# Performance work log

Hardware: AMD Instinct MI355X
Metric: run time of the kernel (lower is better)

## Reference

```python
import jax, jax.numpy as jnp
import numpy as np

B, D, O = 8192, 64, 256

def setup_inputs() -> dict:
    key = jax.random.key(0)
    k1, k2, k3 = jax.random.split(key, 3)
    x = jax.random.normal(k1, (B, D), dtype=jnp.float32)
    centers = jax.random.uniform(k2, (O, 1, D), dtype=jnp.float32)  # RandomUniform(0,1)
    # Original uses Constant(10.0) which saturates exp(-quad) to 0; use small random
    # betas so the quadratic form is in a numerically meaningful range.
    betas = jax.random.normal(k3, (O, D, D), dtype=jnp.float32) * 0.05
    return {"x": x, "centers": centers, "betas": betas}

def reference(x, centers, betas):
    # precision[o] = betas[o] @ betas[o]^T   -> [O, D, D]
    precision = jnp.einsum('ode,ofe->odf', betas, betas)
    # diff[o,b,:] = centers[o] - x[b]        -> [O, B, D]
    diff = centers - x[None, :, :]
    # quad[o,b] = diff[o,b]^T P[o] diff[o,b] -> [O, B]
    quad = jnp.einsum('obd,odf,obf->ob', diff, precision, diff)
    return jnp.exp(-quad).T  # [B, O]
```

## Files before the change

### kernel.cpp

```cpp
#include <hip/hip_runtime.h>
#include <hip/hip_bf16.h>

typedef __bf16 bf16x8 __attribute__((ext_vector_type(8)));
typedef __bf16 bf16x4 __attribute__((ext_vector_type(4)));
typedef float  f32x4  __attribute__((ext_vector_type(4)));

constexpr int Bn = 8192, Dn = 64, On = 256;

__global__ void k_prep_beta(const float* __restrict__ betas, const float* __restrict__ centers,
                            __bf16* __restrict__ bT, float* __restrict__ ncproj) {
    __shared__ float s[64 * 65];
    const int o = blockIdx.x, tid = threadIdx.x;
    const float* bo = betas + (size_t)o * 4096;
    for (int j = tid; j < 1024; j += 256) {
        int d = j >> 4, e = (j & 15) * 4;
        float4 v = ((const float4*)bo)[j];
        s[d * 65 + e + 0] = v.x; s[d * 65 + e + 1] = v.y;
        s[d * 65 + e + 2] = v.z; s[d * 65 + e + 3] = v.w;
    }
    __syncthreads();
    for (int j = tid; j < 1024; j += 256) {
        int e = j >> 4, d = (j & 15) * 4;
        bf16x4 r;
        r[0] = (__bf16)s[(d + 0) * 65 + e]; r[1] = (__bf16)s[(d + 1) * 65 + e];
        r[2] = (__bf16)s[(d + 2) * 65 + e]; r[3] = (__bf16)s[(d + 3) * 65 + e];
        *(bf16x4*)(bT + (size_t)o * 4096 + e * 64 + d) = r;
    }
    if (tid < 64) {
        float acc = 0.f;
        for (int d = 0; d < 64; ++d) acc += s[d * 65 + tid] * centers[o * 64 + d];
        ncproj[o * 64 + tid] = -acc;
    }
}

__global__ __launch_bounds__(256, 4) void k_main(const float* __restrict__ x,
                                                 const __bf16* __restrict__ bT,
                                                 const float* __restrict__ ncproj,
                                                 float* __restrict__ out) {
    __shared__ __align__(16) unsigned char smem[256 * 144];
    __bf16* sX = (__bf16*)smem;
    float*  sQ = (float*)smem;

    const int tid  = threadIdx.x;
    const int w    = tid >> 6, lane = tid & 63;
    const int col  = lane & 15, grp = lane >> 4;
    const int bbase = blockIdx.x * 256;
    const int o     = blockIdx.y * 4 + w;

    const __bf16* bo = bT + (size_t)o * 4096 + (size_t)col * 64 + grp * 8;
    const float*  cp = ncproj + o * 64 + grp * 4;
    bf16x8 A[4][2];
    f32x4  ncp[4];
#pragma unroll
    for (int mi = 0; mi < 4; ++mi) {
        A[mi][0] = *(const bf16x8*)(bo + mi * 16 * 64);
        A[mi][1] = *(const bf16x8*)(bo + mi * 16 * 64 + 32);
        ncp[mi]  = *(const f32x4*)(cp + mi * 16);
    }

#pragma unroll
    for (int it = 0; it < 16; ++it) {
        int i = it * 256 + tid;
        int row = i >> 4, q4 = i & 15;
        float4 v = ((const float4*)(x + (size_t)(bbase + row) * 64))[q4];
        bf16x4 r;
        r[0] = (__bf16)v.x; r[1] = (__bf16)v.y; r[2] = (__bf16)v.z; r[3] = (__bf16)v.w;
        *(bf16x4*)(sX + row * 72 + q4 * 4) = r;
    }
    __syncthreads();

    float qp[16];
#pragma unroll
    for (int n = 0; n < 16; ++n) {
        const __bf16* xr = sX + (n * 16 + col) * 72 + grp * 8;
        bf16x8 x0 = *(const bf16x8*)(xr);
        bf16x8 x1 = *(const bf16x8*)(xr + 32);
        f32x4 qv = {0.f, 0.f, 0.f, 0.f};
#pragma unroll
        for (int mi = 0; mi < 4; ++mi) {
            f32x4 acc = ncp[mi];
            acc = __builtin_amdgcn_mfma_f32_16x16x32_bf16(A[mi][0], x0, acc, 0, 0, 0);
            acc = __builtin_amdgcn_mfma_f32_16x16x32_bf16(A[mi][1], x1, acc, 0, 0, 0);
            qv += acc * acc;
        }
        qp[n] = (qv[0] + qv[1]) + (qv[2] + qv[3]);
    }
    __syncthreads();

#pragma unroll
    for (int n = 0; n < 16; ++n)
        sQ[(n * 16 + col) * 20 + w * 4 + grp] = qp[n];
    __syncthreads();

    const float* qr = sQ + tid * 20;
    f32x4 r;
#pragma unroll
    for (int j = 0; j < 4; ++j) {
        f32x4 v = *(const f32x4*)(qr + j * 4);
        r[j] = __expf(-((v[0] + v[1]) + (v[2] + v[3])));
    }
    *(f32x4*)(out + (size_t)(bbase + tid) * 256 + blockIdx.y * 4) = r;
}

extern "C" void kernel_launch(void* const* d_in, const int* in_sizes, int n_in,
                              void* d_out, int out_size, void* d_ws, size_t ws_size,
                              hipStream_t stream) {
    const float* x       = (const float*)d_in[0];
    const float* centers = (const float*)d_in[1];
    const float* betas   = (const float*)d_in[2];
    float* out = (float*)d_out;

    char* ws = (char*)d_ws;
    __bf16* bT   = (__bf16*)ws;
    float*  ncpj = (float*)(ws + 2 * (1 << 20));

    k_prep_beta<<<dim3(On),               dim3(256), 0, stream>>>(betas, centers, bT, ncpj);
    k_main     <<<dim3(Bn / 256, On / 4), dim3(256), 0, stream>>>(x, bT, ncpj, out);
}
```

Before: 93.25 us.

## Keep x fragments in registers and loop over outputs with double-buffered weights

Each wave now loads and converts its own 128 rows of x straight into MFMA register fragments, so the LDS staging and block barriers are gone. Each block covers 8 outputs instead of 4, halving how often x is re-read across the grid. Weight fragments for successive outputs are double-buffered in registers so their loads overlap the MFMA work. The row reduction now uses cross-lane shuffles, and results are written as single scattered 4-byte stores with a 1 KB stride instead of 16-byte vector stores. That store pattern, plus the higher register use (launch bounds lowered to 2), could offset the savings.

```diff
diff --git a/kernel.cpp b/kernel.cpp
--- a/kernel.cpp
+++ b/kernel.cpp
@@ -33,73 +33,102 @@
     }
 }
 
-__global__ __launch_bounds__(256, 4) void k_main(const float* __restrict__ x,
+struct AFrag { bf16x8 a[4][2]; f32x4 c[4]; };
+
+__device__ __forceinline__ void load_afrag(AFrag& f, const __bf16* aptr, const float* cptr,
+                                           int oi) {
+    const __bf16* p = aptr + (size_t)oi * 4096;
+    const float*  c = cptr + oi * 64;
+#pragma unroll
+    for (int mi = 0; mi < 4; ++mi) {
+        f.a[mi][0] = *(const bf16x8*)(p + mi * 1024);
+        f.a[mi][1] = *(const bf16x8*)(p + mi * 1024 + 32);
+        f.c[mi]    = *(const f32x4*)(c + mi * 16);
+    }
+}
+
+__global__ __launch_bounds__(256, 2) void k_main(const float* __restrict__ x,
                                                  const __bf16* __restrict__ bT,
                                                  const float* __restrict__ ncproj,
                                                  float* __restrict__ out) {
-    __shared__ __align__(16) unsigned char smem[256 * 144];
-    __bf16* sX = (__bf16*)smem;
-    float*  sQ = (float*)smem;
+    const int tid  = threadIdx.x;
+    const int wq   = tid >> 6, lane = tid & 63;
+    const int col  = lane & 15, grp = lane >> 4;
+    const int bbase = blockIdx.x * 512 + wq * 128;
+    const int o0    = blockIdx.y * 8;
 
-    const int tid  = threadIdx.x;
-    const int w    = tid >> 6, lane = tid & 63;
-    const int col  = lane & 15, grp = lane >> 4;
-    const int bbase = blockIdx.x * 256;
-    const int o     = blockIdx.y * 4 + w;
-
-    const __bf16* bo = bT + (size_t)o * 4096 + (size_t)col * 64 + grp * 8;
-    const float*  cp = ncproj + o * 64 + grp * 4;
-    bf16x8 A[4][2];
-    f32x4  ncp[4];
+    bf16x8 xf[8][2];
 #pragma unroll
-    for (int mi = 0; mi < 4; ++mi) {
-        A[mi][0] = *(const bf16x8*)(bo + mi * 16 * 64);
-        A[mi][1] = *(const bf16x8*)(bo + mi * 16 * 64 + 32);
-        ncp[mi]  = *(const f32x4*)(cp + mi * 16);
+    for (int nf = 0; nf < 8; ++nf) {
+        const float* xp = x + (size_t)(bbase + nf * 16 + col) * 64 + grp * 8;
+#pragma unroll
+        for (int ks = 0; ks < 2; ++ks) {
+            float4 v0 = *(const float4*)(xp + ks * 32);
+            float4 v1 = *(const float4*)(xp + ks * 32 + 4);
+            bf16x8 f;
+            f[0] = (__bf16)v0.x; f[1] = (__bf16)v0.y; f[2] = (__bf16)v0.z; f[3] = (__bf16)v0.w;
+            f[4] = (__bf16)v1.x; f[5] = (__bf16)v1.y; f[6] = (__bf16)v1.z; f[7] = (__bf16)v1.w;
+            xf[nf][ks] = f;
+        }
     }
 
-#pragma unroll
-    for (int it = 0; it < 16; ++it) {
-        int i = it * 256 + tid;
-        int row = i >> 4, q4 = i & 15;
-        float4 v = ((const float4*)(x + (size_t)(bbase + row) * 64))[q4];
-        bf16x4 r;
-        r[0] = (__bf16)v.x; r[1] = (__bf16)v.y; r[2] = (__bf16)v.z; r[3] = (__bf16)v.w;
-        *(bf16x4*)(sX + row * 72 + q4 * 4) = r;
-    }
-    __syncthreads();
+    const __bf16* aptr = bT + (size_t)o0 * 4096 + (size_t)col * 64 + grp * 8;
+    const float*  cptr = ncproj + o0 * 64 + grp * 4;
 
-    float qp[16];
-#pragma unroll
-    for (int n = 0; n < 16; ++n) {
-        const __bf16* xr = sX + (n * 16 + col) * 72 + grp * 8;
-        bf16x8 x0 = *(const bf16x8*)(xr);
-        bf16x8 x1 = *(const bf16x8*)(xr + 32);
-        f32x4 qv = {0.f, 0.f, 0.f, 0.f};
-#pragma unroll
-        for (int mi = 0; mi < 4; ++mi) {
-            f32x4 acc = ncp[mi];
-            acc = __builtin_amdgcn_mfma_f32_16x16x32_bf16(A[mi][0], x0, acc, 0, 0, 0);
-            acc = __builtin_amdgcn_mfma_f32_16x16x32_bf16(A[mi][1], x1, acc, 0, 0, 0);
-            qv += acc * acc;
-        }
-        qp[n] = (qv[0] + qv[1]) + (qv[2] + qv[3]);
-    }
-    __syncthreads();
+    AFrag f0, f1;
+    load_afrag(f0, aptr, cptr, 0);
 
 #pragma unroll
-    for (int n = 0; n < 16; ++n)
-        sQ[(n * 16 + col) * 20 + w * 4 + grp] = qp[n];
-    __syncthreads();
-
-    const float* qr = sQ + tid * 20;
-    f32x4 r;
+    for (int oi = 0; oi < 8; oi += 2) {
+        if (oi + 1 < 8) load_afrag(f1, aptr, cptr, oi + 1);
+        {
+            float qp[8];
 #pragma unroll
-    for (int j = 0; j < 4; ++j) {
-        f32x4 v = *(const f32x4*)(qr + j * 4);
-        r[j] = __expf(-((v[0] + v[1]) + (v[2] + v[3])));
+            for (int nf = 0; nf < 8; ++nf) {
+                f32x4 qv = {0.f, 0.f, 0.f, 0.f};
+#pragma unroll
+                for (int mi = 0; mi < 4; ++mi) {
+                    f32x4 acc = f0.c[mi];
+                    acc = __builtin_amdgcn_mfma_f32_16x16x32_bf16(f0.a[mi][0], xf[nf][0], acc, 0, 0, 0);
+                    acc = __builtin_amdgcn_mfma_f32_16x16x32_bf16(f0.a[mi][1], xf[nf][1], acc, 0, 0, 0);
+                    qv += acc * acc;
+                }
+                qp[nf] = (qv[0] + qv[1]) + (qv[2] + qv[3]);
+            }
+#pragma unroll
+            for (int nf = 0; nf < 8; ++nf) {
+                float qs = qp[nf];
+                qs += __shfl_xor(qs, 16, 64);
+                qs += __shfl_xor(qs, 32, 64);
+                if (grp == (nf & 3))
+                    out[(size_t)(bbase + nf * 16 + col) * 256 + (o0 + oi)] = __expf(-qs);
+            }
+        }
+        if (oi + 2 < 8) load_afrag(f0, aptr, cptr, oi + 2);
+        if (oi + 1 < 8) {
+            float qp[8];
+#pragma unroll
+            for (int nf = 0; nf < 8; ++nf) {
+                f32x4 qv = {0.f, 0.f, 0.f, 0.f};
+#pragma unroll
+                for (int mi = 0; mi < 4; ++mi) {
+                    f32x4 acc = f1.c[mi];
+                    acc = __builtin_amdgcn_mfma_f32_16x16x32_bf16(f1.a[mi][0], xf[nf][0], acc, 0, 0, 0);
+                    acc = __builtin_amdgcn_mfma_f32_16x16x32_bf16(f1.a[mi][1], xf[nf][1], acc, 0, 0, 0);
+                    qv += acc * acc;
+                }
+                qp[nf] = (qv[0] + qv[1]) + (qv[2] + qv[3]);
+            }
+#pragma unroll
+            for (int nf = 0; nf < 8; ++nf) {
+                float qs = qp[nf];
+                qs += __shfl_xor(qs, 16, 64);
+                qs += __shfl_xor(qs, 32, 64);
+                if (grp == (nf & 3))
+                    out[(size_t)(bbase + nf * 16 + col) * 256 + (o0 + oi + 1)] = __expf(-qs);
+            }
+        }
     }
-    *(f32x4*)(out + (size_t)(bbase + tid) * 256 + blockIdx.y * 4) = r;
 }
 
 extern "C" void kernel_launch(void* const* d_in, const int* in_sizes, int n_in,
@@ -115,5 +144,5 @@
     float*  ncpj = (float*)(ws + 2 * (1 << 20));
 
     k_prep_beta<<<dim3(On),               dim3(256), 0, stream>>>(betas, centers, bT, ncpj);
-    k_main     <<<dim3(Bn / 256, On / 4), dim3(256), 0, stream>>>(x, bT, ncpj, out);
+    k_main     <<<dim3(Bn / 512, On / 8), dim3(256), 0, stream>>>(x, bT, ncpj, out);
 }
```

Measured after the change: 108.0 us. +15.9%, slower.

## Keep x fragments in registers and loop over eight outputs per block

Applied to the files above, without the earlier changes.

The main kernel now gives each wave its own 64 batch rows. Those rows' x fragments are loaded straight into registers as bf16, so there is no LDS staging. Each block then iterates over 8 output centres, loading each one's beta fragments from global memory, and the grid is halved along O. The LDS transpose and the block syncs are replaced by cross-lane shuffle reductions, and each thread writes 8 contiguous outputs. In exchange, beta fragments are reloaded for each of the 8 centres in every wave, with more register pressure and more shuffles.

```diff
diff --git a/kernel.cpp b/kernel.cpp
--- a/kernel.cpp
+++ b/kernel.cpp
@@ -37,69 +37,63 @@
                                                  const __bf16* __restrict__ bT,
                                                  const float* __restrict__ ncproj,
                                                  float* __restrict__ out) {
-    __shared__ __align__(16) unsigned char smem[256 * 144];
-    __bf16* sX = (__bf16*)smem;
-    float*  sQ = (float*)smem;
+    const int tid  = threadIdx.x;
+    const int wq   = tid >> 6, lane = tid & 63;
+    const int col  = lane & 15, grp = lane >> 4;
+    const int bbase = blockIdx.x * 256 + wq * 64;
+    const int o0    = blockIdx.y * 8;
 
-    const int tid  = threadIdx.x;
-    const int w    = tid >> 6, lane = tid & 63;
-    const int col  = lane & 15, grp = lane >> 4;
-    const int bbase = blockIdx.x * 256;
-    const int o     = blockIdx.y * 4 + w;
-
-    const __bf16* bo = bT + (size_t)o * 4096 + (size_t)col * 64 + grp * 8;
-    const float*  cp = ncproj + o * 64 + grp * 4;
-    bf16x8 A[4][2];
-    f32x4  ncp[4];
+    bf16x8 xf[4][2];
 #pragma unroll
-    for (int mi = 0; mi < 4; ++mi) {
-        A[mi][0] = *(const bf16x8*)(bo + mi * 16 * 64);
-        A[mi][1] = *(const bf16x8*)(bo + mi * 16 * 64 + 32);
-        ncp[mi]  = *(const f32x4*)(cp + mi * 16);
+    for (int nf = 0; nf < 4; ++nf) {
+        const float* xp = x + (size_t)(bbase + nf * 16 + col) * 64 + grp * 8;
+#pragma unroll
+        for (int ks = 0; ks < 2; ++ks) {
+            float4 v0 = *(const float4*)(xp + ks * 32);
+            float4 v1 = *(const float4*)(xp + ks * 32 + 4);
+            bf16x8 f;
+            f[0] = (__bf16)v0.x; f[1] = (__bf16)v0.y; f[2] = (__bf16)v0.z; f[3] = (__bf16)v0.w;
+            f[4] = (__bf16)v1.x; f[5] = (__bf16)v1.y; f[6] = (__bf16)v1.z; f[7] = (__bf16)v1.w;
+            xf[nf][ks] = f;
+        }
     }
 
+    float q8[8];
 #pragma unroll
-    for (int it = 0; it < 16; ++it) {
-        int i = it * 256 + tid;
-        int row = i >> 4, q4 = i & 15;
-        float4 v = ((const float4*)(x + (size_t)(bbase + row) * 64))[q4];
-        bf16x4 r;
-        r[0] = (__bf16)v.x; r[1] = (__bf16)v.y; r[2] = (__bf16)v.z; r[3] = (__bf16)v.w;
-        *(bf16x4*)(sX + row * 72 + q4 * 4) = r;
-    }
-    __syncthreads();
-
-    float qp[16];
-#pragma unroll
-    for (int n = 0; n < 16; ++n) {
-        const __bf16* xr = sX + (n * 16 + col) * 72 + grp * 8;
-        bf16x8 x0 = *(const bf16x8*)(xr);
-        bf16x8 x1 = *(const bf16x8*)(xr + 32);
-        f32x4 qv = {0.f, 0.f, 0.f, 0.f};
+    for (int oi = 0; oi < 8; ++oi) {
+        const __bf16* p = bT + (size_t)(o0 + oi) * 4096 + (size_t)col * 64 + grp * 8;
+        const float*  c = ncproj + (o0 + oi) * 64 + grp * 4;
+        bf16x8 a0[4], a1[4];
+        f32x4  ncp[4];
 #pragma unroll
         for (int mi = 0; mi < 4; ++mi) {
-            f32x4 acc = ncp[mi];
-            acc = __builtin_amdgcn_mfma_f32_16x16x32_bf16(A[mi][0], x0, acc, 0, 0, 0);
-            acc = __builtin_amdgcn_mfma_f32_16x16x32_bf16(A[mi][1], x1, acc, 0, 0, 0);
-            qv += acc * acc;
+            a0[mi]  = *(const bf16x8*)(p + mi * 1024);
+            a1[mi]  = *(const bf16x8*)(p + mi * 1024 + 32);
+            ncp[mi] = *(const f32x4*)(c + mi * 16);
         }
-        qp[n] = (qv[0] + qv[1]) + (qv[2] + qv[3]);
+#pragma unroll
+        for (int nf = 0; nf < 4; ++nf) {
+            f32x4 qv = {0.f, 0.f, 0.f, 0.f};
+#pragma unroll
+            for (int mi = 0; mi < 4; ++mi) {
+                f32x4 acc = ncp[mi];
+                acc = __builtin_amdgcn_mfma_f32_16x16x32_bf16(a0[mi], xf[nf][0], acc, 0, 0, 0);
+                acc = __builtin_amdgcn_mfma_f32_16x16x32_bf16(a1[mi], xf[nf][1], acc, 0, 0, 0);
+                qv += acc * acc;
+            }
+            float qs = (qv[0] + qv[1]) + (qv[2] + qv[3]);
+            qs += __shfl_xor(qs, 16, 64);
+            qs += __shfl_xor(qs, 32, 64);
+            if (grp == nf) q8[oi] = qs;
+        }
     }
-    __syncthreads();
 
+    f32x4 r0, r1;
 #pragma unroll
-    for (int n = 0; n < 16; ++n)
-        sQ[(n * 16 + col) * 20 + w * 4 + grp] = qp[n];
-    __syncthreads();
-
-    const float* qr = sQ + tid * 20;
-    f32x4 r;
-#pragma unroll
-    for (int j = 0; j < 4; ++j) {
-        f32x4 v = *(const f32x4*)(qr + j * 4);
-        r[j] = __expf(-((v[0] + v[1]) + (v[2] + v[3])));
-    }
-    *(f32x4*)(out + (size_t)(bbase + tid) * 256 + blockIdx.y * 4) = r;
+    for (int j = 0; j < 4; ++j) { r0[j] = __expf(-q8[j]); r1[j] = __expf(-q8[4 + j]); }
+    float* op = out + (size_t)(bbase + grp * 16 + col) * 256 + o0;
+    *(f32x4*)op       = r0;
+    *(f32x4*)(op + 4) = r1;
 }
 
 extern "C" void kernel_launch(void* const* d_in, const int* in_sizes, int n_in,
@@ -115,5 +109,5 @@
     float*  ncpj = (float*)(ws + 2 * (1 << 20));
 
     k_prep_beta<<<dim3(On),               dim3(256), 0, stream>>>(betas, centers, bT, ncpj);
-    k_main     <<<dim3(Bn / 256, On / 4), dim3(256), 0, stream>>>(x, bT, ncpj, out);
+    k_main     <<<dim3(Bn / 256, On / 8), dim3(256), 0, stream>>>(x, bT, ncpj, out);
 }
```

Result: slower. 109.6 us (+17.6%).
